# Performance work log

Hardware: AMD Instinct MI355X
Metric: run time of the kernel (lower is better)

## Reference

```python
import jax, jax.numpy as jnp
import numpy as np

B, S, H, NH, NKV, HD, E, I = 1, 2048, 1024, 16, 8, 64, 8, 2048
TOPK = 2
EPS = 1e-6
THETA = 1e6


def setup_inputs() -> dict:
    key = jax.random.key(0)
    ks = jax.random.split(key, 12)
    init = lambda k, shp: jax.random.normal(k, shp, jnp.float32) * 0.02
    hidden_states = jax.random.normal(ks[0], (B, S, H), jnp.float32)
    attention_mask = jnp.ones((B, S), jnp.float32)
    position_ids = jnp.broadcast_to(jnp.arange(S, dtype=jnp.int32), (B, S))
    inv_freq = 1.0 / (THETA ** (jnp.arange(0, HD, 2, dtype=jnp.float32) / HD))
    freqs = jnp.outer(jnp.arange(S, dtype=jnp.float32), inv_freq)  # [S, HD/2]
    emb = jnp.concatenate([freqs, freqs], axis=-1)                  # [S, HD]
    return dict(
        hidden_states=hidden_states,
        attention_mask=attention_mask,
        position_ids=position_ids,
        sin=jnp.sin(emb), cos=jnp.cos(emb),
        wq=init(ks[1], (H, NH * HD)),
        wk=init(ks[2], (H, NKV * HD)),
        wv=init(ks[3], (H, NKV * HD)),
        wo=init(ks[4], (NH * HD, H)),
        ln1=jnp.ones((H,), jnp.float32),
        ln2=jnp.ones((H,), jnp.float32),
        gate_w=init(ks[5], (H, E)),
        w1=init(ks[6], (E, H, I)),
        w3=init(ks[7], (E, H, I)),
        w2=init(ks[8], (E, I, H)),
    )


def _rms_norm(x, w):
    return x * jax.lax.rsqrt(jnp.mean(jnp.square(x), -1, keepdims=True) + EPS) * w


def _rotate_half(x):
    h = x.shape[-1] // 2
    return jnp.concatenate([-x[..., h:], x[..., :h]], axis=-1)


def reference(hidden_states, attention_mask, position_ids, sin, cos,
              wq, wk, wv, wo, ln1, ln2, gate_w, w1, w3, w2):
    x = hidden_states
    # ---- self-attention block ----
    h = _rms_norm(x, ln1)
    q = (h @ wq).reshape(B, S, NH, HD).transpose(0, 2, 1, 3)    # [B,NH,S,HD]
    k = (h @ wk).reshape(B, S, NKV, HD).transpose(0, 2, 1, 3)   # [B,NKV,S,HD]
    v = (h @ wv).reshape(B, S, NKV, HD).transpose(0, 2, 1, 3)
    sb = sin[position_ids][:, None]  # [B,1,S,HD]
    cb = cos[position_ids][:, None]
    q = q * cb + _rotate_half(q) * sb
    k = k * cb + _rotate_half(k) * sb
    rep = NH // NKV
    k = jnp.repeat(k, rep, axis=1)  # GQA repeat -> [B,NH,S,HD]
    v = jnp.repeat(v, rep, axis=1)
    causal = jnp.tril(jnp.ones((S, S), bool))
    mask = causal[None, None] & (attention_mask[:, None, None, :] > 0)
    bias = jnp.where(mask, 0.0, jnp.finfo(jnp.float32).min)
    scale = 1.0 / jnp.sqrt(jnp.float32(HD))
    scores = jnp.einsum('bhqd,bhkd->bhqk', q, k) * scale + bias
    attn = jax.nn.softmax(scores, axis=-1)
    o = jnp.einsum('bhqk,bhkd->bhqd', attn, v)
    o = o.transpose(0, 2, 1, 3).reshape(B, S, NH * HD) @ wo
    x = x + o
    # ---- sparse MoE block (top-2 of E experts, SiLU-gated MLP) ----
    t = _rms_norm(x, ln2).reshape(B * S, H)
    router_logits = t @ gate_w                         # [T,E]
    probs = jax.nn.softmax(router_logits, axis=-1)
    top_w, top_i = jax.lax.top_k(probs, TOPK)          # [T,2]
    top_w = top_w / jnp.sum(top_w, axis=-1, keepdims=True)
    full_w = jnp.sum(jax.nn.one_hot(top_i, E, dtype=t.dtype) * top_w[..., None], axis=1)  # [T,E]
    moe_out = jnp.zeros_like(t)
    for e in range(E):  # fixed small expert count
        ge = jax.nn.silu(t @ w1[e]) * (t @ w3[e])      # [T,I]
        moe_out = moe_out + full_w[:, e:e + 1] * (ge @ w2[e])
    x = x + moe_out.reshape(B, S, H)
    return x
```

## Files before the change

kernel.cpp:

```cpp
#include <hip/hip_runtime.h>

#define S 2048
#define H 1024
#define NH 16
#define NKV 8
#define HD 64
#define NE 8
#define ID 2048

typedef short bf16x8 __attribute__((ext_vector_type(8)));
typedef short bf16x4 __attribute__((ext_vector_type(4)));
typedef float f32x4 __attribute__((ext_vector_type(4)));

__device__ __forceinline__ unsigned short f2bf(float f) {
  unsigned u = __builtin_bit_cast(unsigned, f);
  u += 0x7FFFu + ((u >> 16) & 1u);
  return (unsigned short)(u >> 16);
}
__device__ __forceinline__ float bf2f(unsigned short h) {
  unsigned u = ((unsigned)h) << 16;
  return __builtin_bit_cast(float, u);
}
__device__ __forceinline__ unsigned cvtpk(float a, float b) {
  unsigned r;
  asm("v_cvt_pk_bf16_f32 %0, %1, %2" : "=v"(r) : "v"(a), "v"(b));
  return r;
}

typedef const __attribute__((address_space(1))) unsigned int gas_u32;
typedef __attribute__((address_space(3))) unsigned int las_u32;
__device__ __forceinline__ void gload16(const unsigned short* g, unsigned short* l) {
  __builtin_amdgcn_global_load_lds((gas_u32*)g, (las_u32*)l, 16, 0, 0);
}

__global__ __launch_bounds__(256) void rmsnorm_kernel(const float* __restrict__ x,
                                                      const float* __restrict__ wgt,
                                                      unsigned short* __restrict__ ohi,
                                                      unsigned short* __restrict__ olo) {
  int row = blockIdx.x;
  const float* xr = x + (size_t)row * H;
  int tid = threadIdx.x;
  float v[4];
  float ss = 0.f;
#pragma unroll
  for (int i = 0; i < 4; i++) {
    v[i] = xr[tid + i * 256];
    ss += v[i] * v[i];
  }
#pragma unroll
  for (int off = 1; off < 64; off <<= 1) ss += __shfl_xor(ss, off);
  __shared__ float part[4];
  if ((tid & 63) == 0) part[tid >> 6] = ss;
  __syncthreads();
  float tot = part[0] + part[1] + part[2] + part[3];
  float r = rsqrtf(tot * (1.f / H) + 1e-6f);
#pragma unroll
  for (int i = 0; i < 4; i++) {
    int c = tid + i * 256;
    float vv = v[i] * r * wgt[c];
    size_t o = (size_t)row * H + c;
    unsigned short h_ = f2bf(vv);
    ohi[o] = h_;
    olo[o] = f2bf(vv - bf2f(h_));
  }
}

__global__ __launch_bounds__(256) void rmsnorm_router_kernel(
    const float* __restrict__ x, const float* __restrict__ wgt,
    const float* __restrict__ gw, unsigned short* __restrict__ ohi,
    int* __restrict__ selE, float* __restrict__ selW) {
  int row = blockIdx.x;
  const float* xr = x + (size_t)row * H;
  int tid = threadIdx.x;
  float v[4];
  float ss = 0.f;
#pragma unroll
  for (int i = 0; i < 4; i++) {
    v[i] = xr[tid + i * 256];
    ss += v[i] * v[i];
  }
#pragma unroll
  for (int off = 1; off < 64; off <<= 1) ss += __shfl_xor(ss, off);
  __shared__ float part[4];
  __shared__ float red[4][NE];
  if ((tid & 63) == 0) part[tid >> 6] = ss;
  __syncthreads();
  float tot = part[0] + part[1] + part[2] + part[3];
  float r = rsqrtf(tot * (1.f / H) + 1e-6f);
  float acc[NE];
#pragma unroll
  for (int e = 0; e < NE; e++) acc[e] = 0.f;
#pragma unroll
  for (int i = 0; i < 4; i++) {
    int c = tid + i * 256;
    float vv = v[i] * r * wgt[c];
    ohi[(size_t)row * H + c] = f2bf(vv);
    const float4* gp = (const float4*)(gw + (size_t)c * NE);
    float4 g0 = gp[0], g1 = gp[1];
    acc[0] += vv * g0.x;
    acc[1] += vv * g0.y;
    acc[2] += vv * g0.z;
    acc[3] += vv * g0.w;
    acc[4] += vv * g1.x;
    acc[5] += vv * g1.y;
    acc[6] += vv * g1.z;
    acc[7] += vv * g1.w;
  }
#pragma unroll
  for (int off = 1; off < 64; off <<= 1) {
#pragma unroll
    for (int e = 0; e < NE; e++) acc[e] += __shfl_xor(acc[e], off);
  }
  if ((tid & 63) == 0) {
#pragma unroll
    for (int e = 0; e < NE; e++) red[tid >> 6][e] = acc[e];
  }
  __syncthreads();
  if (tid == 0) {
    float lg[NE];
#pragma unroll
    for (int e = 0; e < NE; e++) lg[e] = red[0][e] + red[1][e] + red[2][e] + red[3][e];
    int e1 = 0;
#pragma unroll
    for (int e = 1; e < NE; e++)
      if (lg[e] > lg[e1]) e1 = e;
    int e2 = -1;
#pragma unroll
    for (int e = 0; e < NE; e++)
      if (e != e1 && (e2 < 0 || lg[e] > lg[e2])) e2 = e;
    float w1v = 1.f / (1.f + __expf(lg[e2] - lg[e1]));
    selE[row] = e1 | (e2 << 8);
    selW[row * 2] = w1v;
    selW[row * 2 + 1] = 1.f - w1v;
  }
}

__global__ __launch_bounds__(256) void assign_kernel(const int* __restrict__ selE,
                                                     int* __restrict__ cnt,
                                                     int* __restrict__ offs,
                                                     int* __restrict__ tmap,
                                                     int* __restrict__ idxb,
                                                     int* __restrict__ tokslot) {
  int tid = threadIdx.x;
  __shared__ int sc[256][NE];
  int pack[8];
  int hist[NE];
#pragma unroll
// ... 1 lines not shown
#pragma unroll
  for (int i = 0; i < 8; i++) {
    pack[i] = selE[tid * 8 + i];
    hist[pack[i] & 255]++;
    hist[(pack[i] >> 8) & 255]++;
  }
#pragma unroll
  for (int e = 0; e < NE; e++) sc[tid][e] = hist[e];
  __syncthreads();
  for (int off = 1; off < 256; off <<= 1) {
    int add[NE];
    bool has = tid >= off;
    if (has) {
#pragma unroll
      for (int e = 0; e < NE; e++) add[e] = sc[tid - off][e];
    }
    __syncthreads();
    if (has) {
#pragma unroll
      for (int e = 0; e < NE; e++) sc[tid][e] += add[e];
    }
    __syncthreads();
  }
  int offsL[NE];
  {
    int a = 0;
#pragma unroll
    for (int e = 0; e < NE; e++) {
      offsL[e] = a;
      a += sc[255][e];
    }
  }
  if (tid == 0) {
    int t = 0;
    for (int e = 0; e < NE; e++) {
      int totE = sc[255][e];
      offs[e] = offsL[e];
      cnt[e] = totE;
      int nt = (totE + 127) >> 7;
      for (int i = 0; i < nt; i++) tmap[t++] = (e << 16) | i;
    }
    offs[NE] = offsL[NE - 1] + sc[255][NE - 1];
    tmap[63] = t;
  }
  int run[NE];
#pragma unroll
  for (int e = 0; e < NE; e++) run[e] = sc[tid][e] - hist[e];
#pragma unroll
  for (int i = 0; i < 8; i++) {
    int tok = tid * 8 + i;
    int e1 = pack[i] & 255, e2 = (pack[i] >> 8) & 255;
    int p1 = run[e1]++;
    idxb[e1 * S + p1] = tok;
    int p2 = run[e2]++;
    idxb[e2 * S + p2] = tok;
    tokslot[tok * 2] = offsL[e1] + p1;
    tokslot[tok * 2 + 1] = offsL[e2] + p2;
  }
}

__global__ __launch_bounds__(256) void moe_gather_kernel(const float* __restrict__ moeP,
                                                         const int* __restrict__ tokslot,
                                                         const float* __restrict__ selW,
                                                         float* __restrict__ out) {
  int tok = blockIdx.x;
  int c = threadIdx.x * 4;
  int s0 = tokslot[tok * 2], s1 = tokslot[tok * 2 + 1];
  float w0 = selW[tok * 2], w1 = selW[tok * 2 + 1];
  const float* P0 = moeP;
  const float* P1 = moeP + (size_t)4096 * 1024;
  float4 a0 = *(const float4*)(P0 + (size_t)s0 * 1024 + c);
  float4 b0 = *(const float4*)(P1 + (size_t)s0 * 1024 + c);
  float4 a1 = *(const float4*)(P0 + (size_t)s1 * 1024 + c);
  float4 b1 = *(const float4*)(P1 + (size_t)s1 * 1024 + c);
  float* op = out + (size_t)tok * 1024 + c;
  float4 o = *(float4*)op;
  o.x += w0 * (a0.x + b0.x) + w1 * (a1.x + b1.x);
  o.y += w0 * (a0.y + b0.y) + w1 * (a1.y + b1.y);
  o.z += w0 * (a0.z + b0.z) + w1 * (a1.z + b1.z);
  o.w += w0 * (a0.w + b0.w) + w1 * (a1.w + b1.w);
  *(float4*)op = o;
}

template <bool LO>
__device__ __forceinline__ void tconv_tile128(const float* __restrict__ src,
                                              unsigned short* __restrict__ hi,
                                              unsigned short* __restrict__ lo, int K, int N,
                                              int nt, int kt, float (*tile)[65]) {
  int tid = threadIdx.x;
  int wv = tid >> 6, ln = tid & 63;
  const float* sb = src + (size_t)(kt * 128) * N + nt * 64 + ln;
#pragma unroll 8
  for (int rr = 0; rr < 32; rr++) {
    int r = rr * 4 + wv;
    tile[r][ln] = sb[(size_t)r * N];
  }
  __syncthreads();
  int seg = tid & 15;
  int rq = tid >> 4;
#pragma unroll
  for (int it = 0; it < 4; it++) {
    int row = it * 16 + rq;
    int cs = seg * 8;
    size_t dbase = (size_t)(nt * 64 + row) * K + kt * 128 + cs;
    unsigned short th[8], tl[8];
#pragma unroll
    for (int i = 0; i < 8; i++) {
      float vv = tile[cs + i][row];
      unsigned short h_ = f2bf(vv);
      th[i] = h_;
      if (LO) tl[i] = f2bf(vv - bf2f(h_));
    }
    *(bf16x8*)(hi + dbase) = *(bf16x8*)&th[0];
    if (LO) *(bf16x8*)(lo + dbase) = *(bf16x8*)&tl[0];
  }
}

__global__ __launch_bounds__(256, 4) void tconv_attn_kernel(
    const float* __restrict__ wq, const float* __restrict__ wk, const float* __restrict__ wv,
    const float* __restrict__ wo, unsigned short* __restrict__ wqkvT_hi,
    unsigned short* __restrict__ wqkvT_lo, unsigned short* __restrict__ woT_hi,
    unsigned short* __restrict__ woT_lo) {
  __shared__ float tile[128][65];
  int u = blockIdx.x;
  const float* src;
  unsigned short *hi, *lo;
  int N, local;
  if (u < 128) {
    src = wq; hi = wqkvT_hi; lo = wqkvT_lo; N = 1024; local = u;
  } else if (u < 192) {
    src = wk; hi = wqkvT_hi + (size_t)1024 * 1024; lo = wqkvT_lo + (size_t)1024 * 1024; N = 512; local = u - 128;
  } else if (u < 256) {
    src = wv; hi = wqkvT_hi + (size_t)1536 * 1024; lo = wqkvT_lo + (size_t)1536 * 1024; N = 512; local = u - 192;
  } else {
    src = wo; hi = woT_hi; lo = woT_lo; N = 1024; local = u - 256;
  }
  int ntc = N >> 6;
  int nt = local % ntc, kt = local / ntc;
  tconv_tile128<true>(src, hi, lo, 1024, N, nt, kt, tile);
}

__global__ __launch_bounds__(256, 4) void tconv_w13_kernel(const float* __restrict__ w1,
                                                           const float* __restrict__ w3,
                                                           unsigned short* __restrict__ w1T,
                                                           unsigned short* __restrict__ w3T) {
  __shared__ float tile[128][65];
  int b = blockIdx.z;
  const float* src = (b < 8) ? w1 + (size_t)b * 1024 * 2048 : w3 + (size_t)(b - 8) * 1024 * 2048;
  unsigned short* hi = (b < 8) ? w1T + (size_t)b * 2048 * 1024 : w3T + (size_t)(b - 8) * 2048 * 1024;
  tconv_tile128<false>(src, hi, nullptr, 1024, 2048, blockIdx.x, blockIdx.y, tile);
}

__global__ __launch_bounds__(256, 4) void tconv_w2_kernel(const float* __restrict__ w2,
                                                          unsigned short* __restrict__ w2T) {
  __shared__ float tile[128][65];
  int b = blockIdx.z;
  tconv_tile128<false>(w2 + (size_t)b * 2048 * 1024, w2T + (size_t)b * 1024 * 2048, nullptr, 2048,
                       1024, blockIdx.x, blockIdx.y, tile);
}

template <int MODE>
__global__ __launch_bounds__(256, 4) void gemm_kernel(
    const unsigned short* __restrict__ Ah, const unsigned short* __restrict__ Al,
    const unsigned short* __restrict__ Bh, const unsigned short* __restrict__ Bl,
    float* __restrict__ C, float* __restrict__ C2, unsigned short* __restrict__ Gout,
    const float* __restrict__ resid, const int* __restrict__ idx,
    const int* __restrict__ cnt, const int* __restrict__ offs,
    const int* __restrict__ tmap, int N, int K) {
  constexpr int BM = (MODE <= 1) ? 64 : 128;
  constexpr int NI = BM / 32;
  int n0 = blockIdx.x * 64, m0, e = 0;
  int ce = 0, gbase = 0;
  if (MODE >= 2) {
    int ntiles = tmap[63];
    if ((int)blockIdx.y >= ntiles) return;
    int packed = tmap[blockIdx.y];
    e = packed >> 16;
    m0 = (packed & 0xffff) * 128;
    ce = cnt[e];
    gbase = offs[e];
  } else {
    m0 = blockIdx.y * BM;
  }
  const unsigned short* bhp = Bh;
  const unsigned short* blp = Bl;
  if (MODE == 2) {
    bhp += (size_t)e * 2048 * 1024;
    blp += (size_t)e * 2048 * 1024;
  }
  if (MODE == 3) bhp += (size_t)e * 1024 * 2048;

  __shared__ __align__(16) unsigned short tAh[BM * 64];
  __shared__ __align__(16) unsigned short tAl[MODE <= 1 ? BM * 64 : 8];
  __shared__ __align__(16) unsigned short tBh[64 * 64];
  __shared__ __align__(16) unsigned short tBl[MODE <= 2 ? 64 * 64 : 8];

  int tid = threadIdx.x, w = tid >> 6, lane = tid & 63;
  int lr = lane & 15, g = lane >> 4;
  int rloc = lane >> 3, slotg = (lane & 7) ^ rloc;
  int wm = w >> 1, wn = w & 1;

  unsigned aOff[NI], bOff[2];
#pragma unroll
  for (int cc = 0; cc < NI; cc++) {
    int rr = (w * NI + cc) * 8 + rloc;
    if (MODE == 2) {
      int gr = m0 + rr;
      if (gr > ce - 1) gr = ce - 1;
      int tok = idx[e * S + gr];
      aOff[cc] = (unsigned)(tok * K + slotg * 8);
    } else if (MODE == 3) {
      int gr = gbase + m0 + rr;
      if (gr > 4095) gr = 4095;
      aOff[cc] = (unsigned)(gr * K + slotg * 8);
    } else {
      aOff[cc] = (unsigned)((m0 + rr) * K + slotg * 8);
    }
  }
#pragma unroll
  for (int cc = 0; cc < 2; cc++) {
    int rr = (w * 2 + cc) * 8 + rloc;
    bOff[cc] = (unsigned)((n0 + rr) * K + slotg * 8);
  }

  f32x4 acc[NI][2], acc2[NI][2];
#pragma unroll
  for (int i = 0; i < NI; i++)
#pragma unroll
    for (int j = 0; j < 2; j++) {
      acc[i][j] = f32x4{0.f, 0.f, 0.f, 0.f};
      if (MODE == 2) acc2[i][j] = f32x4{0.f, 0.f, 0.f, 0.f};
    }

  int kbeg = 0, kend = K;
  if (MODE == 3) {
    kbeg = (int)blockIdx.z * (K >> 1);
    kend = kbeg + (K >> 1);
  }
  for (int k0 = kbeg; k0 < kend; k0 += 64) {
    __syncthreads();
#pragma unroll
    for (int cc = 0; cc < NI; cc++) {
      int cb = (w * NI + cc) * 512;
      gload16(Ah + aOff[cc] + k0, &tAh[cb]);
      if (MODE <= 1) gload16(Al + aOff[cc] + k0, &tAl[cb]);
    }
#pragma unroll
    for (int cc = 0; cc < 2; cc++) {
      int cb = (w * 2 + cc) * 512;
      gload16(bhp + bOff[cc] + k0, &tBh[cb]);
      if (MODE <= 2) gload16(blp + bOff[cc] + k0, &tBl[cb]);
    }
    __syncthreads();
    bf16x8 fah[NI][2], fal[NI][2];
#pragma unroll
    for (int i = 0; i < NI; i++) {
      int ar = wm * (BM / 2) + i * 16 + lr;
#pragma unroll
      for (int kk = 0; kk < 2; kk++) {
        int off = ar * 64 + (((kk * 4 + g) ^ (ar & 7)) * 8);
        fah[i][kk] = *(const bf16x8*)&tAh[off];
        if (MODE <= 1) fal[i][kk] = *(const bf16x8*)&tAl[off];
      }
    }
#pragma unroll
    for (int j = 0; j < 2; j++) {
      int br = wn * 32 + j * 16 + lr;
      bf16x8 fbh[2], fbl[2];
#pragma unroll
      for (int kk = 0; kk < 2; kk++) {
        int off = br * 64 + (((kk * 4 + g) ^ (br & 7)) * 8);
        fbh[kk] = *(const bf16x8*)&tBh[off];
        if (MODE <= 2) fbl[kk] = *(const bf16x8*)&tBl[off];
      }
#pragma unroll
      for (int i = 0; i < NI; i++) {
#pragma unroll
        for (int kk = 0; kk < 2; kk++) {
          acc[i][j] = __builtin_amdgcn_mfma_f32_16x16x32_bf16(fah[i][kk], fbh[kk], acc[i][j], 0, 0, 0);
          if (MODE <= 1) {
            acc[i][j] = __builtin_amdgcn_mfma_f32_16x16x32_bf16(fah[i][kk], fbl[kk], acc[i][j], 0, 0, 0);
            acc[i][j] = __builtin_amdgcn_mfma_f32_16x16x32_bf16(fal[i][kk], fbh[kk], acc[i][j], 0, 0, 0);
          }
          if (MODE == 2)
            acc2[i][j] = __builtin_amdgcn_mfma_f32_16x16x32_bf16(fah[i][kk], fbl[kk], acc2[i][j], 0, 0, 0);
        }
      }
    }
  }
#pragma unroll
  for (int i = 0; i < NI; i++)
#pragma unroll
    for (int j = 0; j < 2; j++)
#pragma unroll
      for (int r = 0; r < 4; r++) {
        int grow = wm * (BM / 2) + i * 16 + g * 4 + r;
        int gcol = n0 + wn * 32 + j * 16 + lr;
        float v = acc[i][j][r];
        if (MODE == 0) {
          C[(size_t)(m0 + grow) * N + gcol] = v;
        } else if (MODE == 1) {
          float o = v + resid[(size_t)(m0 + grow) * N + gcol];
          C[(size_t)(m0 + grow) * N + gcol] = o;
          C2[(size_t)(m0 + grow) * N + gcol] = o;
        } else if (MODE == 2) {
          if (m0 + grow < ce) {
            float g3 = acc2[i][j][r];
            float sg = v / (1.f + __expf(-v));
            Gout[(size_t)(gbase + m0 + grow) * 2048 + gcol] = f2bf(sg * g3);
          }
        } else {
          if (m0 + grow < ce) {
            C[(size_t)blockIdx.z * 4096 * 1024 + (size_t)(gbase + m0 + grow) * 1024 + gcol] = v;
          }
        }
      }
}

__global__ __launch_bounds__(256) void rope_kernel(
    const float* __restrict__ qkv, const float* __restrict__ sinb,
    const float* __restrict__ cosb, const int* __restrict__ pos,
    unsigned short* __restrict__ qhi, unsigned short* __restrict__ qlo,
    unsigned short* __restrict__ khi, unsigned short* __restrict__ klo) {
  int i = blockIdx.x * 256 + threadIdx.x;
  int d = i & 31;
  int s = (i >> 5) & 2047;
  int hh = i >> 16;
  int p = pos[s];
  float c0 = cosb[p * HD + d], c1 = cosb[p * HD + d + 32];
  float s0 = sinb[p * HD + d], s1 = sinb[p * HD + d + 32];
  const float* srcb = qkv + (size_t)s * 2048;
  if (hh < NH) {
    float x0 = srcb[hh * HD + d], x1 = srcb[hh * HD + d + 32];
    float r0 = (x0 * c0 - x1 * s0) * 0.125f;
    float r1 = (x1 * c1 + x0 * s1) * 0.125f;
    size_t o = ((size_t)hh * S + s) * HD + d;
    unsigned short h0 = f2bf(r0), h1 = f2bf(r1);
    qhi[o] = h0;
    qlo[o] = f2bf(r0 - bf2f(h0));
    qhi[o + 32] = h1;
    qlo[o + 32] = f2bf(r1 - bf2f(h1));
  } else {
    int hk = hh - NH;
    float x0 = srcb[1024 + hk * HD + d], x1 = srcb[1024 + hk * HD + d + 32];
    float r0 = x0 * c0 - x1 * s0;
    float r1 = x1 * c1 + x0 * s1;
    size_t o = ((size_t)hk * S + s) * HD + d;
    unsigned short h0 = f2bf(r0), h1 = f2bf(r1);
    khi[o] = h0;
    klo[o] = f2bf(r0 - bf2f(h0));
    khi[o + 32] = h1;
    klo[o + 32] = f2bf(r1 - bf2f(h1));
  }
}

__global__ __launch_bounds__(256) void vtrans_kernel(const float* __restrict__ qkv,
                                                     unsigned short* __restrict__ vThi,
                                                     unsigned short* __restrict__ vTlo) {
  int st = blockIdx.x, hk = blockIdx.y;
  __shared__ float tile[64][65];
  int tid = threadIdx.x;
  int r = tid >> 2, seg = (tid & 3) * 16;
  const float* src = qkv + (size_t)(st * 64 + r) * 2048 + 1536 + hk * HD + seg;
#pragma unroll
  for (int i = 0; i < 16; i += 4) {
    float4 a = *(const float4*)(src + i);
    tile[r][seg + i] = a.x;
    tile[r][seg + i + 1] = a.y;
    tile[r][seg + i + 2] = a.z;
    tile[r][seg + i + 3] = a.w;
  }
  __syncthreads();
  int d = tid >> 2, ss = (tid & 3) * 16;
  unsigned short th[16], tl[16];
#pragma unroll
  for (int i = 0; i < 16; i++) {
    float vv = tile[ss + i][d];
    unsigned short h_ = f2bf(vv);
    th[i] = h_;
    tl[i] = f2bf(vv - bf2f(h_));
  }
  size_t dst = ((size_t)hk * HD + d) * S + st * 64 + ss;
  *(bf16x8*)(vThi + dst) = *(bf16x8*)&th[0];
  *(bf16x8*)(vThi + dst + 8) = *(bf16x8*)&th[8];
  *(bf16x8*)(vTlo + dst) = *(bf16x8*)&tl[0];
  *(bf16x8*)(vTlo + dst + 8) = *(bf16x8*)&tl[8];
}

#define FSWZ(row, byteoff) ((byteoff) ^ (((row) & 7) << 4))

__global__ __launch_bounds__(256, 4) void flash_kernel(
    const unsigned short* __restrict__ qhi, const unsigned short* __restrict__ qlo,
    const unsigned short* __restrict__ khip, const unsigned short* __restrict__ klop,
    const unsigned short* __restrict__ vthip, const unsigned short* __restrict__ vtlop,
    const float* __restrict__ amask, float* __restrict__ po, float* __restrict__ pm,
    float* __restrict__ pl) {
  int u = blockIdx.x;
  int r_ = u >> 8, base = u & 255;
  int qt = (base + r_ * 8) & 31;
  int head = ((base >> 5) & 7) | ((r_ & 1) << 3);
  int z = r_ >> 1;
  int tid = threadIdx.x;
  int w = tid >> 6, lane = tid & 63;
  int lr = lane & 15, g = lane >> 4;
  int rloc = lane >> 3, slotg = (lane & 7) ^ rloc;

  __shared__ __align__(16) unsigned short Khi[64 * 64];
  __shared__ __align__(16) unsigned short Klo[64 * 64];
  __shared__ __align__(16) unsigned short Vhi[64 * 64];
  __shared__ __align__(16) unsigned short Vlo[64 * 64];
  __shared__ __align__(16) unsigned short Pbuf[4][16 * 64];

  int qrow = qt * 64 + w * 16 + lr;
  bf16x8 qh[2], ql[2];
  {
    const unsigned short* qb = qhi + ((size_t)head * S + qrow) * HD;
    const unsigned short* qb2 = qlo + ((size_t)head * S + qrow) * HD;
    qh[0] = *(const bf16x8*)(qb + g * 8);
    qh[1] = *(const bf16x8*)(qb + 32 + g * 8);
    ql[0] = *(const bf16x8*)(qb2 + g * 8);
    ql[1] = *(const bf16x8*)(qb2 + 32 + g * 8);
  }

  f32x4 oacc[4];
#pragma unroll
  for (int dg = 0; dg < 4; dg++) oacc[dg] = f32x4{0.f, 0.f, 0.f, 0.f};
  float m = -1e30f, l = 0.f;

  const unsigned short* kbh = khip + (size_t)(head >> 1) * S * HD;
  const unsigned short* kbl = klop + (size_t)(head >> 1) * S * HD;
  const unsigned short* vbh = vthip + (size_t)(head >> 1) * HD * S;
  const unsigned short* vbl = vtlop + (size_t)(head >> 1) * HD * S;
  char* pbase = (char*)Pbuf[w];

  int nblk = qt + 1;
  int b0 = (z * nblk) >> 1, b1 = ((z + 1) * nblk) >> 1;

  for (int kb = b0; kb < b1; kb++) {
    int kv0 = kb * 64;
    __syncthreads();
#pragma unroll
    for (int cc = 0; cc < 2; cc++) {
      int c = w * 2 + cc;
      int r = c * 8 + rloc;
      gload16(kbh + (size_t)(kv0 + r) * HD + slotg * 8, &Khi[c * 512]);
      gload16(kbl + (size_t)(kv0 + r) * HD + slotg * 8, &Klo[c * 512]);
      gload16(vbh + (size_t)r * S + kv0 + slotg * 8, &Vhi[c * 512]);
      gload16(vbl + (size_t)r * S + kv0 + slotg * 8, &Vlo[c * 512]);
    }
    unsigned long long vm = __ballot(amask[kv0 + lane] > 0.f);
    __syncthreads();

    f32x4 sacc[4];
#pragma unroll
    for (int c = 0; c < 4; c++) sacc[c] = f32x4{0.f, 0.f, 0.f, 0.f};
#pragma unroll
    for (int c = 0; c < 4; c++) {
#pragma unroll
      for (int kc = 0; kc < 2; kc++) {
        int row = c * 16 + lr;
        int bo = FSWZ(row, row * 128 + kc * 64 + g * 16);
        bf16x8 khf = *(const bf16x8*)((char*)Khi + bo);
        bf16x8 klf = *(const bf16x8*)((char*)Klo + bo);
        sacc[c] = __builtin_amdgcn_mfma_f32_16x16x32_bf16(khf, qh[kc], sacc[c], 0, 0, 0);
        sacc[c] = __builtin_amdgcn_mfma_f32_16x16x32_bf16(khf, ql[kc], sacc[c], 0, 0, 0);
        sacc[c] = __builtin_amdgcn_mfma_f32_16x16x32_bf16(klf, qh[kc], sacc[c], 0, 0, 0);
      }
    }
    int qloc = w * 16 + lr;
// ... 87 lines not shown
  }

  size_t pb = (size_t)(qt * 16 + head) * 2 + z;
  int row = w * 16 + lr;
  if (g == 0) {
    pm[pb * 64 + row] = m;
    pl[pb * 64 + row] = l;
  }
  float* pob = po + pb * 4096 + (size_t)row * 64;
#pragma unroll
  for (int dg = 0; dg < 4; dg++) {
    float4 v4 = {oacc[dg][0], oacc[dg][1], oacc[dg][2], oacc[dg][3]};
    *(float4*)(pob + dg * 16 + 4 * g) = v4;
  }
}

__global__ __launch_bounds__(256) void combine_kernel(const float* __restrict__ po,
                                                      const float* __restrict__ pm,
                                                      const float* __restrict__ pl,
                                                      unsigned short* __restrict__ ohi,
                                                      unsigned short* __restrict__ olo) {
  int qt = blockIdx.x, head = blockIdx.y;
  int r = threadIdx.x >> 2, dg = (threadIdx.x & 3) * 16;
  size_t base = (size_t)(qt * 16 + head) * 2;
  float m0v = pm[base * 64 + r], m1v = pm[(base + 1) * 64 + r];
  float l0 = pl[base * 64 + r], l1 = pl[(base + 1) * 64 + r];
  float M = fmaxf(m0v, m1v);
  float w0 = __expf(m0v - M), w1 = __expf(m1v - M);
  float inv = 1.f / (w0 * l0 + w1 * l1);
  const float* p0 = po + base * 4096 + (size_t)r * 64 + dg;
  const float* p1 = po + (base + 1) * 4096 + (size_t)r * 64 + dg;
  unsigned short th[16], tl[16];
#pragma unroll
  for (int i = 0; i < 16; i += 4) {
    float4 a = *(const float4*)(p0 + i);
    float4 b = *(const float4*)(p1 + i);
    float vv[4] = {(w0 * a.x + w1 * b.x) * inv, (w0 * a.y + w1 * b.y) * inv,
                   (w0 * a.z + w1 * b.z) * inv, (w0 * a.w + w1 * b.w) * inv};
#pragma unroll
    for (int j = 0; j < 4; j++) {
      unsigned short h_ = f2bf(vv[j]);
      th[i + j] = h_;
      tl[i + j] = f2bf(vv[j] - bf2f(h_));
    }
  }
  size_t ob = (size_t)(qt * 64 + r) * 1024 + head * 64 + dg;
  *(bf16x8*)(ohi + ob) = *(bf16x8*)&th[0];
  *(bf16x8*)(ohi + ob + 8) = *(bf16x8*)&th[8];
  *(bf16x8*)(olo + ob) = *(bf16x8*)&tl[0];
  *(bf16x8*)(olo + ob + 8) = *(bf16x8*)&tl[8];
}

extern "C" void kernel_launch(void* const* d_in, const int* in_sizes, int n_in,
                              void* d_out, int out_size, void* d_ws, size_t ws_size,
                              hipStream_t stream) {
  const float* x = (const float*)d_in[0];
  const float* amask = (const float*)d_in[1];
  const int* pos = (const int*)d_in[2];
  const float* sinb = (const float*)d_in[3];
  const float* cosb = (const float*)d_in[4];
  const float* wq = (const float*)d_in[5];
  const float* wk = (const float*)d_in[6];
  const float* wv = (const float*)d_in[7];
  const float* wo = (const float*)d_in[8];
  const float* ln1 = (const float*)d_in[9];
  const float* ln2 = (const float*)d_in[10];
  const float* gw = (const float*)d_in[11];
  const float* w1 = (const float*)d_in[12];
  const float* w3 = (const float*)d_in[13];
  const float* w2 = (const float*)d_in[14];
  float* out = (float*)d_out;

  char* ws = (char*)d_ws;
  const size_t MB = 1024 * 1024;
  float* x2 = (float*)(ws + 0 * MB);
  unsigned short* t_bf = (unsigned short*)(ws + 8 * MB);
  int* cnt = (int*)(ws + 12 * MB);
  int* offs = cnt + 16;
  int* tmap = cnt + 32;
  int* idxb = cnt + 128;
  int* selE = idxb + 16384;
  int* tokslot = selE + 2048;
  float* selW = (float*)(tokslot + 4096);
  unsigned short* G = (unsigned short*)(ws + 13 * MB);
  unsigned short* w1T = (unsigned short*)(ws + 29 * MB);
  unsigned short* w3T = (unsigned short*)(ws + 61 * MB);
  unsigned short* w2T = (unsigned short*)(ws + 29 * MB);
  float* moeP = (float*)(ws + 61 * MB);
  float* qkv = (float*)(ws + 13 * MB);
  float* po = (float*)(ws + 13 * MB);
  unsigned short* wqkvT_hi = (unsigned short*)(ws + 29 * MB);
  unsigned short* wqkvT_lo = (unsigned short*)(ws + 33 * MB);
  unsigned short* woT_hi = (unsigned short*)(ws + 37 * MB);
  unsigned short* woT_lo = (unsigned short*)(ws + 39 * MB);
  unsigned short* h_hi = (unsigned short*)(ws + 41 * MB);
  unsigned short* h_lo = (unsigned short*)(ws + 45 * MB);
  unsigned short* q_hi = (unsigned short*)(ws + 49 * MB);
  unsigned short* q_lo = (unsigned short*)(ws + 53 * MB);
  unsigned short* k_hi = (unsigned short*)(ws + 57 * MB);
  unsigned short* k_lo = (unsigned short*)(ws + 59 * MB);
  unsigned short* vT_hi = (unsigned short*)(ws + 61 * MB);
  unsigned short* vT_lo = (unsigned short*)(ws + 63 * MB);
  unsigned short* o_hi = (unsigned short*)(ws + 65 * MB);
  unsigned short* o_lo = (unsigned short*)(ws + 69 * MB);
  float* pm = (float*)(ws + 73 * MB);
  float* pl = (float*)(ws + 74 * MB);

  rmsnorm_kernel<<<S, 256, 0, stream>>>(x, ln1, h_hi, h_lo);
  tconv_attn_kernel<<<384, 256, 0, stream>>>(wq, wk, wv, wo, wqkvT_hi, wqkvT_lo, woT_hi, woT_lo);

  gemm_kernel<0><<<dim3(32, 32, 1), 256, 0, stream>>>(h_hi, h_lo, wqkvT_hi, wqkvT_lo, qkv, nullptr,
                                                      nullptr, nullptr, nullptr, nullptr, nullptr,
                                                      nullptr, 2048, 1024);
  rope_kernel<<<6144, 256, 0, stream>>>(qkv, sinb, cosb, pos, q_hi, q_lo, k_hi, k_lo);
  vtrans_kernel<<<dim3(32, 8), 256, 0, stream>>>(qkv, vT_hi, vT_lo);
  flash_kernel<<<dim3(1024, 1, 1), 256, 0, stream>>>(q_hi, q_lo, k_hi, k_lo, vT_hi, vT_lo, amask,
                                                     po, pm, pl);
  combine_kernel<<<dim3(32, 16), 256, 0, stream>>>(po, pm, pl, o_hi, o_lo);
  gemm_kernel<1><<<dim3(16, 32, 1), 256, 0, stream>>>(o_hi, o_lo, woT_hi, woT_lo, x2, out, nullptr,
                                                      x, nullptr, nullptr, nullptr, nullptr, 1024,
                                                      1024);
  rmsnorm_router_kernel<<<S, 256, 0, stream>>>(x2, ln2, gw, t_bf, selE, selW);
  assign_kernel<<<1, 256, 0, stream>>>(selE, cnt, offs, tmap, idxb, tokslot);

  tconv_w13_kernel<<<dim3(32, 8, 16), 256, 0, stream>>>(w1, w3, w1T, w3T);
  gemm_kernel<2><<<dim3(32, 40, 1), 256, 0, stream>>>(t_bf, nullptr, w1T, w3T, nullptr, nullptr, G,
                                                      nullptr, idxb, cnt, offs, tmap, 2048, 1024);
  tconv_w2_kernel<<<dim3(16, 16, 8), 256, 0, stream>>>(w2, w2T);
  gemm_kernel<3><<<dim3(16, 40, 2), 256, 0, stream>>>(G, nullptr, w2T, nullptr, moeP, nullptr,
                                                      nullptr, nullptr, idxb, cnt, offs, tmap, 1024,
                                                      2048);
  moe_gather_kernel<<<S, 256, 0, stream>>>(moeP, tokslot, selW, out);
}
```

Baseline: 289.5 us.

## Fuse independent kernels into interleaved multi-role launches to overlap work

Merges rmsnorm with the attention weight transpose-convert into one interleaved launch, and rope with the V transpose into another. It also fuses the output-projection GEMM with the w1/w3 expert weight conversion, interleaving blocks so memory-bound conversion overlaps compute. The workspace layout is reshuffled so buffers with overlapping lifetimes do not collide. This removes launch gaps and tail underutilisation, at the cost of divergent block roles, higher shared memory per block and a fixed 64x64 tile for the Wo GEMM.

```diff
diff --git a/kernel.cpp b/kernel.cpp
--- a/kernel.cpp
+++ b/kernel.cpp
@@ -33,36 +33,261 @@
   __builtin_amdgcn_global_load_lds((gas_u32*)g, (las_u32*)l, 16, 0, 0);
 }
 
-__global__ __launch_bounds__(256) void rmsnorm_kernel(const float* __restrict__ x,
-                                                      const float* __restrict__ wgt,
-                                                      unsigned short* __restrict__ ohi,
-                                                      unsigned short* __restrict__ olo) {
-  int row = blockIdx.x;
-  const float* xr = x + (size_t)row * H;
+template <bool LO>
+__device__ __forceinline__ void tconv_tile128(const float* __restrict__ src,
+                                              unsigned short* __restrict__ hi,
+                                              unsigned short* __restrict__ lo, int K, int N,
+                                              int nt, int kt, float (*tile)[65]) {
   int tid = threadIdx.x;
-  float v[4];
-  float ss = 0.f;
-#pragma unroll
-  for (int i = 0; i < 4; i++) {
-    v[i] = xr[tid + i * 256];
-    ss += v[i] * v[i];
-  }
-#pragma unroll
-  for (int off = 1; off < 64; off <<= 1) ss += __shfl_xor(ss, off);
+  int wv = tid >> 6, ln = tid & 63;
+  const float* sb = src + (size_t)(kt * 128) * N + nt * 64 + ln;
+#pragma unroll 8
+  for (int rr = 0; rr < 32; rr++) {
+    int r = rr * 4 + wv;
+    tile[r][ln] = sb[(size_t)r * N];
+  }
+  __syncthreads();
+  int seg = tid & 15;
+  int rq = tid >> 4;
+#pragma unroll
+  for (int it = 0; it < 4; it++) {
+    int row = it * 16 + rq;
+    int cs = seg * 8;
+    size_t dbase = (size_t)(nt * 64 + row) * K + kt * 128 + cs;
+    unsigned short th[8], tl[8];
+#pragma unroll
+    for (int i = 0; i < 8; i++) {
+      float vv = tile[cs + i][row];
+      unsigned short h_ = f2bf(vv);
+      th[i] = h_;
+      if (LO) tl[i] = f2bf(vv - bf2f(h_));
+    }
+    *(bf16x8*)(hi + dbase) = *(bf16x8*)&th[0];
+    if (LO) *(bf16x8*)(lo + dbase) = *(bf16x8*)&tl[0];
+  }
+}
+
+__global__ __launch_bounds__(256) void prep_kernel(
+    const float* __restrict__ x, const float* __restrict__ ln1,
+    unsigned short* __restrict__ h_hi, unsigned short* __restrict__ h_lo,
+    const float* __restrict__ wq, const float* __restrict__ wk, const float* __restrict__ wv,
+    const float* __restrict__ wo, unsigned short* __restrict__ wqkvT_hi,
+    unsigned short* __restrict__ wqkvT_lo, unsigned short* __restrict__ woT_hi,
+    unsigned short* __restrict__ woT_lo) {
+  __shared__ float tile[128][65];
   __shared__ float part[4];
-  if ((tid & 63) == 0) part[tid >> 6] = ss;
-  __syncthreads();
-  float tot = part[0] + part[1] + part[2] + part[3];
-  float r = rsqrtf(tot * (1.f / H) + 1e-6f);
-#pragma unroll
-  for (int i = 0; i < 4; i++) {
-    int c = tid + i * 256;
-    float vv = v[i] * r * wgt[c];
-    size_t o = (size_t)row * H + c;
-    unsigned short h_ = f2bf(vv);
-    ohi[o] = h_;
-    olo[o] = f2bf(vv - bf2f(h_));
-  }
+  int u = blockIdx.x, grp = u / 19, slot = u % 19;
+  int tid = threadIdx.x;
+  if (slot < 16) {
+    int row = grp * 16 + slot;
+    const float* xr = x + (size_t)row * H;
+    float v[4];
+    float ss = 0.f;
+#pragma unroll
+    for (int i = 0; i < 4; i++) {
+      v[i] = xr[tid + i * 256];
+      ss += v[i] * v[i];
+    }
+#pragma unroll
+    for (int off = 1; off < 64; off <<= 1) ss += __shfl_xor(ss, off);
+    if ((tid & 63) == 0) part[tid >> 6] = ss;
+    __syncthreads();
+    float tot = part[0] + part[1] + part[2] + part[3];
+    float r = rsqrtf(tot * (1.f / H) + 1e-6f);
+#pragma unroll
+    for (int i = 0; i < 4; i++) {
+      int c = tid + i * 256;
+      float vv = v[i] * r * ln1[c];
+      size_t o = (size_t)row * H + c;
+      unsigned short h_ = f2bf(vv);
+      h_hi[o] = h_;
+      h_lo[o] = f2bf(vv - bf2f(h_));
+    }
+  } else {
+    int local = grp * 3 + (slot - 16);
+    const float* src;
+    unsigned short *hi, *lo;
+    int N, l2;
+    if (local < 128) {
+      src = wq; hi = wqkvT_hi; lo = wqkvT_lo; N = 1024; l2 = local;
+    } else if (local < 192) {
+      src = wk; hi = wqkvT_hi + (size_t)1024 * 1024; lo = wqkvT_lo + (size_t)1024 * 1024; N = 512; l2 = local - 128;
+    } else if (local < 256) {
+      src = wv; hi = wqkvT_hi + (size_t)1536 * 1024; lo = wqkvT_lo + (size_t)1536 * 1024; N = 512; l2 = local - 192;
+    } else {
+      src = wo; hi = woT_hi; lo = woT_lo; N = 1024; l2 = local - 256;
+    }
+    int ntc = N >> 6;
+    int nt = l2 % ntc, kt = l2 / ntc;
+    tconv_tile128<true>(src, hi, lo, 1024, N, nt, kt, tile);
+  }
+}
+
+__global__ __launch_bounds__(256) void rv_kernel(
+    const float* __restrict__ qkv, const float* __restrict__ sinb,
+    const float* __restrict__ cosb, const int* __restrict__ pos,
+    unsigned short* __restrict__ qhi, unsigned short* __restrict__ qlo,
+    unsigned short* __restrict__ khi, unsigned short* __restrict__ klo,
+    unsigned short* __restrict__ vThi, unsigned short* __restrict__ vTlo) {
+  __shared__ float tile[64][65];
+  int u = blockIdx.x, grp = u / 25, slot = u % 25;
+  int tid = threadIdx.x;
+  if (slot == 0) {
+    int st = grp & 31, hk = grp >> 5;
+    int r = tid >> 2, seg = (tid & 3) * 16;
+    const float* src = qkv + (size_t)(st * 64 + r) * 2048 + 1536 + hk * HD + seg;
+#pragma unroll
+    for (int i = 0; i < 16; i += 4) {
+      float4 a = *(const float4*)(src + i);
+      tile[r][seg + i] = a.x;
+      tile[r][seg + i + 1] = a.y;
+      tile[r][seg + i + 2] = a.z;
+      tile[r][seg + i + 3] = a.w;
+    }
+    __syncthreads();
+    int d = tid >> 2, ss = (tid & 3) * 16;
+    unsigned short th[16], tl[16];
+#pragma unroll
+    for (int i = 0; i < 16; i++) {
+      float vv = tile[ss + i][d];
+      unsigned short h_ = f2bf(vv);
+      th[i] = h_;
+      tl[i] = f2bf(vv - bf2f(h_));
+    }
+    size_t dst = ((size_t)hk * HD + d) * S + st * 64 + ss;
+    *(bf16x8*)(vThi + dst) = *(bf16x8*)&th[0];
+    *(bf16x8*)(vThi + dst + 8) = *(bf16x8*)&th[8];
+    *(bf16x8*)(vTlo + dst) = *(bf16x8*)&tl[0];
+    *(bf16x8*)(vTlo + dst + 8) = *(bf16x8*)&tl[8];
+  } else {
+    int i = (grp * 24 + slot - 1) * 256 + tid;
+    int d = i & 31;
+    int s = (i >> 5) & 2047;
+    int hh = i >> 16;
+    int p = pos[s];
+    float c0 = cosb[p * HD + d], c1 = cosb[p * HD + d + 32];
+    float s0 = sinb[p * HD + d], s1 = sinb[p * HD + d + 32];
+    const float* srcb = qkv + (size_t)s * 2048;
+    if (hh < NH) {
+      float x0 = srcb[hh * HD + d], x1 = srcb[hh * HD + d + 32];
+      float r0 = (x0 * c0 - x1 * s0) * 0.125f;
+      float r1 = (x1 * c1 + x0 * s1) * 0.125f;
+      size_t o = ((size_t)hh * S + s) * HD + d;
+      unsigned short h0 = f2bf(r0), h1 = f2bf(r1);
+      qhi[o] = h0;
+      qlo[o] = f2bf(r0 - bf2f(h0));
+      qhi[o + 32] = h1;
+      qlo[o + 32] = f2bf(r1 - bf2f(h1));
+    } else {
+      int hk = hh - NH;
+      float x0 = srcb[1024 + hk * HD + d], x1 = srcb[1024 + hk * HD + d + 32];
+      float r0 = x0 * c0 - x1 * s0;
+      float r1 = x1 * c1 + x0 * s1;
+      size_t o = ((size_t)hk * S + s) * HD + d;
+      unsigned short h0 = f2bf(r0), h1 = f2bf(r1);
+      khi[o] = h0;
+      klo[o] = f2bf(r0 - bf2f(h0));
+      khi[o + 32] = h1;
+      klo[o + 32] = f2bf(r1 - bf2f(h1));
+    }
+  }
+}
+
+__global__ __launch_bounds__(256, 4) void gemm1_w13_kernel(
+    const unsigned short* __restrict__ oh, const unsigned short* __restrict__ ol,
+    const unsigned short* __restrict__ woh, const unsigned short* __restrict__ wol,
+    float* __restrict__ x2, float* __restrict__ out, const float* __restrict__ resid,
+    const float* __restrict__ w1, const float* __restrict__ w3,
+    unsigned short* __restrict__ w1T, unsigned short* __restrict__ w3T) {
+  __shared__ __align__(16) char smem[33280];
+  int u = blockIdx.x, grp = u / 9, slot = u % 9;
+  int tid = threadIdx.x;
+  if (slot != 0) {
+    int t = grp * 8 + slot - 1;
+    int b = t >> 8, rem = t & 255, kt = rem >> 5, nt = rem & 31;
+    const float* src = (b < 8) ? w1 + (size_t)b * 1024 * 2048 : w3 + (size_t)(b - 8) * 1024 * 2048;
+    unsigned short* hi = (b < 8) ? w1T + (size_t)b * 2048 * 1024 : w3T + (size_t)(b - 8) * 2048 * 1024;
+    tconv_tile128<false>(src, hi, nullptr, 1024, 2048, nt, kt, (float(*)[65])smem);
+    return;
+  }
+  int g = grp;
+  int bx = g & 15, by = g >> 4;
+  unsigned short* tAh = (unsigned short*)smem;
+  unsigned short* tAl = tAh + 4096;
+  unsigned short* tBh = tAl + 4096;
+  unsigned short* tBl = tBh + 4096;
+  int n0 = bx * 64, m0 = by * 64;
+  int w = tid >> 6, lane = tid & 63;
+  int lr = lane & 15, gq = lane >> 4;
+  int rloc = lane >> 3, slotg = (lane & 7) ^ rloc;
+  int wm = w >> 1, wn = w & 1;
+  unsigned aOff[2], bOff[2];
+#pragma unroll
+  for (int cc = 0; cc < 2; cc++) {
+    int rr = (w * 2 + cc) * 8 + rloc;
+    aOff[cc] = (unsigned)((m0 + rr) * 1024 + slotg * 8);
+    bOff[cc] = (unsigned)((n0 + rr) * 1024 + slotg * 8);
+  }
+  f32x4 acc[2][2];
+#pragma unroll
+  for (int i = 0; i < 2; i++)
+#pragma unroll
+    for (int j = 0; j < 2; j++) acc[i][j] = f32x4{0.f, 0.f, 0.f, 0.f};
+  for (int k0 = 0; k0 < 1024; k0 += 64) {
+    __syncthreads();
+#pragma unroll
+    for (int cc = 0; cc < 2; cc++) {
+      int cb = (w * 2 + cc) * 512;
+      gload16(oh + aOff[cc] + k0, &tAh[cb]);
+      gload16(ol + aOff[cc] + k0, &tAl[cb]);
+      gload16(woh + bOff[cc] + k0, &tBh[cb]);
+      gload16(wol + bOff[cc] + k0, &tBl[cb]);
+    }
+    __syncthreads();
+    bf16x8 fah[2][2], fal[2][2];
+#pragma unroll
+    for (int i = 0; i < 2; i++) {
+      int ar = wm * 32 + i * 16 + lr;
+#pragma unroll
+      for (int kk = 0; kk < 2; kk++) {
+        int off = ar * 64 + (((kk * 4 + gq) ^ (ar & 7)) * 8);
+        fah[i][kk] = *(const bf16x8*)&tAh[off];
+        fal[i][kk] = *(const bf16x8*)&tAl[off];
+      }
+    }
+#pragma unroll
+    for (int j = 0; j < 2; j++) {
+      int br = wn * 32 + j * 16 + lr;
+      bf16x8 fbh[2], fbl[2];
+#pragma unroll
+      for (int kk = 0; kk < 2; kk++) {
+        int off = br * 64 + (((kk * 4 + gq) ^ (br & 7)) * 8);
+        fbh[kk] = *(const bf16x8*)&tBh[off];
+        fbl[kk] = *(const bf16x8*)&tBl[off];
+      }
+#pragma unroll
+      for (int i = 0; i < 2; i++) {
+#pragma unroll
+        for (int kk = 0; kk < 2; kk++) {
+          acc[i][j] = __builtin_amdgcn_mfma_f32_16x16x32_bf16(fah[i][kk], fbh[kk], acc[i][j], 0, 0, 0);
+          acc[i][j] = __builtin_amdgcn_mfma_f32_16x16x32_bf16(fah[i][kk], fbl[kk], acc[i][j], 0, 0, 0);
+          acc[i][j] = __builtin_amdgcn_mfma_f32_16x16x32_bf16(fal[i][kk], fbh[kk], acc[i][j], 0, 0, 0);
+        }
+      }
+    }
+  }
+#pragma unroll
+  for (int i = 0; i < 2; i++)
+#pragma unroll
+    for (int j = 0; j < 2; j++)
+#pragma unroll
+      for (int r = 0; r < 4; r++) {
+        int grow = wm * 32 + i * 16 + gq * 4 + r;
+        int gcol = n0 + wn * 32 + j * 16 + lr;
+        float o = acc[i][j][r] + resid[(size_t)(m0 + grow) * 1024 + gcol];
+        x2[(size_t)(m0 + grow) * 1024 + gcol] = o;
+        out[(size_t)(m0 + grow) * 1024 + gcol] = o;
+      }
 }
 
 __global__ __launch_bounds__(256) void rmsnorm_router_kernel(
@@ -230,75 +455,6 @@
   *(float4*)op = o;
 }
 
-template <bool LO>
-__device__ __forceinline__ void tconv_tile128(const float* __restrict__ src,
-                                              unsigned short* __restrict__ hi,
-                                              unsigned short* __restrict__ lo, int K, int N,
-                                              int nt, int kt, float (*tile)[65]) {
-  int tid = threadIdx.x;
-  int wv = tid >> 6, ln = tid & 63;
-  const float* sb = src + (size_t)(kt * 128) * N + nt * 64 + ln;
-#pragma unroll 8
-  for (int rr = 0; rr < 32; rr++) {
-    int r = rr * 4 + wv;
-    tile[r][ln] = sb[(size_t)r * N];
-  }
-  __syncthreads();
-  int seg = tid & 15;
-  int rq = tid >> 4;
-#pragma unroll
-  for (int it = 0; it < 4; it++) {
-    int row = it * 16 + rq;
-    int cs = seg * 8;
-    size_t dbase = (size_t)(nt * 64 + row) * K + kt * 128 + cs;
-    unsigned short th[8], tl[8];
-#pragma unroll
-    for (int i = 0; i < 8; i++) {
-      float vv = tile[cs + i][row];
-      unsigned short h_ = f2bf(vv);
-      th[i] = h_;
-      if (LO) tl[i] = f2bf(vv - bf2f(h_));
-    }
-    *(bf16x8*)(hi + dbase) = *(bf16x8*)&th[0];
-    if (LO) *(bf16x8*)(lo + dbase) = *(bf16x8*)&tl[0];
-  }
-}
-
-__global__ __launch_bounds__(256, 4) void tconv_attn_kernel(
-    const float* __restrict__ wq, const float* __restrict__ wk, const float* __restrict__ wv,
-    const float* __restrict__ wo, unsigned short* __restrict__ wqkvT_hi,
-    unsigned short* __restrict__ wqkvT_lo, unsigned short* __restrict__ woT_hi,
-    unsigned short* __restrict__ woT_lo) {
-  __shared__ float tile[128][65];
-  int u = blockIdx.x;
-  const float* src;
-  unsigned short *hi, *lo;
-  int N, local;
-  if (u < 128) {
-    src = wq; hi = wqkvT_hi; lo = wqkvT_lo; N = 1024; local = u;
-  } else if (u < 192) {
-    src = wk; hi = wqkvT_hi + (size_t)1024 * 1024; lo = wqkvT_lo + (size_t)1024 * 1024; N = 512; local = u - 128;
-  } else if (u < 256) {
-    src = wv; hi = wqkvT_hi + (size_t)1536 * 1024; lo = wqkvT_lo + (size_t)1536 * 1024; N = 512; local = u - 192;
-  } else {
-    src = wo; hi = woT_hi; lo = woT_lo; N = 1024; local = u - 256;
-  }
-  int ntc = N >> 6;
-  int nt = local % ntc, kt = local / ntc;
-  tconv_tile128<true>(src, hi, lo, 1024, N, nt, kt, tile);
-}
-
-__global__ __launch_bounds__(256, 4) void tconv_w13_kernel(const float* __restrict__ w1,
-                                                           const float* __restrict__ w3,
-                                                           unsigned short* __restrict__ w1T,
-                                                           unsigned short* __restrict__ w3T) {
-  __shared__ float tile[128][65];
-  int b = blockIdx.z;
-  const float* src = (b < 8) ? w1 + (size_t)b * 1024 * 2048 : w3 + (size_t)(b - 8) * 1024 * 2048;
-  unsigned short* hi = (b < 8) ? w1T + (size_t)b * 2048 * 1024 : w3T + (size_t)(b - 8) * 2048 * 1024;
-  tconv_tile128<false>(src, hi, nullptr, 1024, 2048, blockIdx.x, blockIdx.y, tile);
-}
-
 __global__ __launch_bounds__(256, 4) void tconv_w2_kernel(const float* __restrict__ w2,
                                                           unsigned short* __restrict__ w2T) {
   __shared__ float tile[128][65];
@@ -311,9 +467,8 @@
 __global__ __launch_bounds__(256, 4) void gemm_kernel(
     const unsigned short* __restrict__ Ah, const unsigned short* __restrict__ Al,
     const unsigned short* __restrict__ Bh, const unsigned short* __restrict__ Bl,
-    float* __restrict__ C, float* __restrict__ C2, unsigned short* __restrict__ Gout,
-    const float* __restrict__ resid, const int* __restrict__ idx,
-    const int* __restrict__ cnt, const int* __restrict__ offs,
+    float* __restrict__ C, unsigned short* __restrict__ Gout,
+    const int* __restrict__ idx, const int* __restrict__ cnt, const int* __restrict__ offs,
     const int* __restrict__ tmap, int N, int K) {
   constexpr int BM = (MODE <= 1) ? 64 : 128;
   constexpr int NI = BM / 32;
@@ -447,92 +602,18 @@
         float v = acc[i][j][r];
         if (MODE == 0) {
           C[(size_t)(m0 + grow) * N + gcol] = v;
-        } else if (MODE == 1) {
-          float o = v + resid[(size_t)(m0 + grow) * N + gcol];
-          C[(size_t)(m0 + grow) * N + gcol] = o;
-          C2[(size_t)(m0 + grow) * N + gcol] = o;
         } else if (MODE == 2) {
           if (m0 + grow < ce) {
             float g3 = acc2[i][j][r];
             float sg = v / (1.f + __expf(-v));
             Gout[(size_t)(gbase + m0 + grow) * 2048 + gcol] = f2bf(sg * g3);
           }
-        } else {
+        } else if (MODE == 3) {
           if (m0 + grow < ce) {
             C[(size_t)blockIdx.z * 4096 * 1024 + (size_t)(gbase + m0 + grow) * 1024 + gcol] = v;
           }
         }
       }
-}
-
-__global__ __launch_bounds__(256) void rope_kernel(
-    const float* __restrict__ qkv, const float* __restrict__ sinb,
-    const float* __restrict__ cosb, const int* __restrict__ pos,
-    unsigned short* __restrict__ qhi, unsigned short* __restrict__ qlo,
-    unsigned short* __restrict__ khi, unsigned short* __restrict__ klo) {
-  int i = blockIdx.x * 256 + threadIdx.x;
-  int d = i & 31;
-  int s = (i >> 5) & 2047;
-  int hh = i >> 16;
-  int p = pos[s];
-  float c0 = cosb[p * HD + d], c1 = cosb[p * HD + d + 32];
-  float s0 = sinb[p * HD + d], s1 = sinb[p * HD + d + 32];
-  const float* srcb = qkv + (size_t)s * 2048;
-  if (hh < NH) {
-    float x0 = srcb[hh * HD + d], x1 = srcb[hh * HD + d + 32];
-    float r0 = (x0 * c0 - x1 * s0) * 0.125f;
-    float r1 = (x1 * c1 + x0 * s1) * 0.125f;
-    size_t o = ((size_t)hh * S + s) * HD + d;
-    unsigned short h0 = f2bf(r0), h1 = f2bf(r1);
-    qhi[o] = h0;
-    qlo[o] = f2bf(r0 - bf2f(h0));
-    qhi[o + 32] = h1;
-    qlo[o + 32] = f2bf(r1 - bf2f(h1));
-  } else {
-    int hk = hh - NH;
-    float x0 = srcb[1024 + hk * HD + d], x1 = srcb[1024 + hk * HD + d + 32];
-    float r0 = x0 * c0 - x1 * s0;
-    float r1 = x1 * c1 + x0 * s1;
-    size_t o = ((size_t)hk * S + s) * HD + d;
-    unsigned short h0 = f2bf(r0), h1 = f2bf(r1);
-    khi[o] = h0;
-    klo[o] = f2bf(r0 - bf2f(h0));
-    khi[o + 32] = h1;
-    klo[o + 32] = f2bf(r1 - bf2f(h1));
-  }
-}
-
-__global__ __launch_bounds__(256) void vtrans_kernel(const float* __restrict__ qkv,
-                                                     unsigned short* __restrict__ vThi,
-                                                     unsigned short* __restrict__ vTlo) {
-  int st = blockIdx.x, hk = blockIdx.y;
-  __shared__ float tile[64][65];
-  int tid = threadIdx.x;
-  int r = tid >> 2, seg = (tid & 3) * 16;
-  const float* src = qkv + (size_t)(st * 64 + r) * 2048 + 1536 + hk * HD + seg;
-#pragma unroll
-  for (int i = 0; i < 16; i += 4) {
-    float4 a = *(const float4*)(src + i);
-    tile[r][seg + i] = a.x;
-    tile[r][seg + i + 1] = a.y;
-    tile[r][seg + i + 2] = a.z;
-    tile[r][seg + i + 3] = a.w;
-  }
-  __syncthreads();
-  int d = tid >> 2, ss = (tid & 3) * 16;
-  unsigned short th[16], tl[16];
-#pragma unroll
-  for (int i = 0; i < 16; i++) {
-    float vv = tile[ss + i][d];
-    unsigned short h_ = f2bf(vv);
-    th[i] = h_;
-    tl[i] = f2bf(vv - bf2f(h_));
-  }
-  size_t dst = ((size_t)hk * HD + d) * S + st * 64 + ss;
-  *(bf16x8*)(vThi + dst) = *(bf16x8*)&th[0];
-  *(bf16x8*)(vThi + dst + 8) = *(bf16x8*)&th[8];
-  *(bf16x8*)(vTlo + dst) = *(bf16x8*)&tl[0];
-  *(bf16x8*)(vTlo + dst + 8) = *(bf16x8*)&tl[8];
 }
 
 #define FSWZ(row, byteoff) ((byteoff) ^ (((row) & 7) << 4))
@@ -786,53 +867,47 @@
   int* selE = idxb + 16384;
   int* tokslot = selE + 2048;
   float* selW = (float*)(tokslot + 4096);
+  unsigned short* o_hi = (unsigned short*)(ws + 13 * MB);
+  unsigned short* o_lo = (unsigned short*)(ws + 17 * MB);
   unsigned short* G = (unsigned short*)(ws + 13 * MB);
+  float* qkv = (float*)(ws + 13 * MB);
   unsigned short* w1T = (unsigned short*)(ws + 29 * MB);
   unsigned short* w3T = (unsigned short*)(ws + 61 * MB);
   unsigned short* w2T = (unsigned short*)(ws + 29 * MB);
   float* moeP = (float*)(ws + 61 * MB);
-  float* qkv = (float*)(ws + 13 * MB);
-  float* po = (float*)(ws + 13 * MB);
-  unsigned short* wqkvT_hi = (unsigned short*)(ws + 29 * MB);
-  unsigned short* wqkvT_lo = (unsigned short*)(ws + 33 * MB);
-  unsigned short* woT_hi = (unsigned short*)(ws + 37 * MB);
-  unsigned short* woT_lo = (unsigned short*)(ws + 39 * MB);
-  unsigned short* h_hi = (unsigned short*)(ws + 41 * MB);
-  unsigned short* h_lo = (unsigned short*)(ws + 45 * MB);
-  unsigned short* q_hi = (unsigned short*)(ws + 49 * MB);
-  unsigned short* q_lo = (unsigned short*)(ws + 53 * MB);
-  unsigned short* k_hi = (unsigned short*)(ws + 57 * MB);
-  unsigned short* k_lo = (unsigned short*)(ws + 59 * MB);
-  unsigned short* vT_hi = (unsigned short*)(ws + 61 * MB);
-  unsigned short* vT_lo = (unsigned short*)(ws + 63 * MB);
-  unsigned short* o_hi = (unsigned short*)(ws + 65 * MB);
-  unsigned short* o_lo = (unsigned short*)(ws + 69 * MB);
-  float* pm = (float*)(ws + 73 * MB);
-  float* pl = (float*)(ws + 74 * MB);
-
-  rmsnorm_kernel<<<S, 256, 0, stream>>>(x, ln1, h_hi, h_lo);
-  tconv_attn_kernel<<<384, 256, 0, stream>>>(wq, wk, wv, wo, wqkvT_hi, wqkvT_lo, woT_hi, woT_lo);
-
+  float* po = (float*)(ws + 29 * MB);
+  float* pm = (float*)(ws + 45 * MB);
+  float* pl = (float*)(ws + 46 * MB);
+  unsigned short* wqkvT_hi = (unsigned short*)(ws + 47 * MB);
+  unsigned short* wqkvT_lo = (unsigned short*)(ws + 51 * MB);
+  unsigned short* h_hi = (unsigned short*)(ws + 55 * MB);
+  unsigned short* h_lo = (unsigned short*)(ws + 59 * MB);
+  unsigned short* q_hi = (unsigned short*)(ws + 63 * MB);
+  unsigned short* q_lo = (unsigned short*)(ws + 67 * MB);
+  unsigned short* k_hi = (unsigned short*)(ws + 71 * MB);
+  unsigned short* k_lo = (unsigned short*)(ws + 73 * MB);
+  unsigned short* vT_hi = (unsigned short*)(ws + 75 * MB);
+  unsigned short* vT_lo = (unsigned short*)(ws + 77 * MB);
+  unsigned short* woT_hi = (unsigned short*)(ws + 93 * MB);
+  unsigned short* woT_lo = (unsigned short*)(ws + 95 * MB);
+
+  prep_kernel<<<2432, 256, 0, stream>>>(x, ln1, h_hi, h_lo, wq, wk, wv, wo, wqkvT_hi, wqkvT_lo,
+                                        woT_hi, woT_lo);
   gemm_kernel<0><<<dim3(32, 32, 1), 256, 0, stream>>>(h_hi, h_lo, wqkvT_hi, wqkvT_lo, qkv, nullptr,
-                                                      nullptr, nullptr, nullptr, nullptr, nullptr,
-                                                      nullptr, 2048, 1024);
-  rope_kernel<<<6144, 256, 0, stream>>>(qkv, sinb, cosb, pos, q_hi, q_lo, k_hi, k_lo);
-  vtrans_kernel<<<dim3(32, 8), 256, 0, stream>>>(qkv, vT_hi, vT_lo);
+                                                      nullptr, nullptr, nullptr, nullptr, 2048,
+                                                      1024);
+  rv_kernel<<<6400, 256, 0, stream>>>(qkv, sinb, cosb, pos, q_hi, q_lo, k_hi, k_lo, vT_hi, vT_lo);
   flash_kernel<<<dim3(1024, 1, 1), 256, 0, stream>>>(q_hi, q_lo, k_hi, k_lo, vT_hi, vT_lo, amask,
                                                      po, pm, pl);
   combine_kernel<<<dim3(32, 16), 256, 0, stream>>>(po, pm, pl, o_hi, o_lo);
-  gemm_kernel<1><<<dim3(16, 32, 1), 256, 0, stream>>>(o_hi, o_lo, woT_hi, woT_lo, x2, out, nullptr,
-                                                      x, nullptr, nullptr, nullptr, nullptr, 1024,
-                                                      1024);
+  gemm1_w13_kernel<<<4608, 256, 0, stream>>>(o_hi, o_lo, woT_hi, woT_lo, x2, out, x, w1, w3, w1T,
+                                             w3T);
   rmsnorm_router_kernel<<<S, 256, 0, stream>>>(x2, ln2, gw, t_bf, selE, selW);
   assign_kernel<<<1, 256, 0, stream>>>(selE, cnt, offs, tmap, idxb, tokslot);
-
-  tconv_w13_kernel<<<dim3(32, 8, 16), 256, 0, stream>>>(w1, w3, w1T, w3T);
-  gemm_kernel<2><<<dim3(32, 40, 1), 256, 0, stream>>>(t_bf, nullptr, w1T, w3T, nullptr, nullptr, G,
-                                                      nullptr, idxb, cnt, offs, tmap, 2048, 1024);
+  gemm_kernel<2><<<dim3(32, 40, 1), 256, 0, stream>>>(t_bf, nullptr, w1T, w3T, nullptr, G, idxb,
+                                                      cnt, offs, tmap, 2048, 1024);
   tconv_w2_kernel<<<dim3(16, 16, 8), 256, 0, stream>>>(w2, w2T);
   gemm_kernel<3><<<dim3(16, 40, 2), 256, 0, stream>>>(G, nullptr, w2T, nullptr, moeP, nullptr,
-                                                      nullptr, nullptr, idxb, cnt, offs, tmap, 1024,
-                                                      2048);
+                                                      idxb, cnt, offs, tmap, 1024, 2048);
   moe_gather_kernel<<<S, 256, 0, stream>>>(moeP, tokslot, selW, out);
 }
```

Result: faster. 281.3 us (-2.8%).
